# Kernel optimization log

Hardware: AMD Instinct MI355X
Metric: run time of the kernel (lower is better)

Reference implementation:

```python
import jax, jax.numpy as jnp
import numpy as np

B, T, D, K = 8, 1024, 512, 1024
PRECISION = 0.1


def setup_inputs() -> dict:
    key = jax.random.key(0)
    kx, kc = jax.random.split(key)
    x = jax.random.normal(kx, (B, T, D), dtype=jnp.float32)
    codebook = jax.random.normal(kc, (K, D), dtype=jnp.float32)
    precision = PRECISION * jnp.ones((1,), dtype=jnp.float32)
    return {"x": x, "codebook": codebook, "precision": precision}


def reference(x, codebook, precision):
    # score[b,t,k] = -sum_d (x[b,t,d] - codebook[k,d])^2
    x_sq = jnp.sum(x * x, axis=-1, keepdims=True)            # [B,T,1]
    c_sq = jnp.sum(codebook * codebook, axis=-1)              # [K]
    xc = jnp.einsum('btd,kd->btk', x, codebook)               # [B,T,K] GEMM
    score = -(x_sq - 2.0 * xc + c_sq)                         # [B,T,K]
    return precision * score
```

## Files before the change

### kernel.cpp

```cpp
#include <hip/hip_runtime.h>

typedef unsigned short u16;
typedef __attribute__((ext_vector_type(8))) short short8;
typedef __attribute__((ext_vector_type(4))) float f32x4;

typedef void gvoid_t __attribute__((address_space(1)));
typedef void lvoid_t __attribute__((address_space(3)));

#define M_DIM 8192
#define N_DIM 1024
#define K_DIM 512

__device__ __forceinline__ void async_copy16(const void* g, void* l) {
  __builtin_amdgcn_global_load_lds((gvoid_t*)g, (lvoid_t*)l, 16, 0, 0);
}

__device__ __forceinline__ unsigned bf16bits(float v) {
  union { float f; unsigned u; } c; c.f = v;
  return (c.u + 0x7FFFu + ((c.u >> 16) & 1u)) >> 16;
}

__global__ __launch_bounds__(256) void cvt_sq_kernel(
    const float* __restrict__ x, const float* __restrict__ cb,
    u16* __restrict__ xb, u16* __restrict__ cbb,
    float* __restrict__ xsq, float* __restrict__ csq) {
  int row = blockIdx.x * 4 + (threadIdx.x >> 6);
  int lane = threadIdx.x & 63;
  const float* src; u16* dst; float* sq;
  if (row < M_DIM) {
    src = x + (size_t)row * K_DIM; dst = xb + (size_t)row * K_DIM; sq = xsq + row;
  } else {
    int r = row - M_DIM;
    src = cb + (size_t)r * K_DIM; dst = cbb + (size_t)r * K_DIM; sq = csq + r;
  }
  const float4* s4 = (const float4*)src;
  float4 v0 = s4[lane];
  float4 v1 = s4[lane + 64];
  float s = v0.x * v0.x + v0.y * v0.y + v0.z * v0.z + v0.w * v0.w +
            v1.x * v1.x + v1.y * v1.y + v1.z * v1.z + v1.w * v1.w;
  uint2* d2 = (uint2*)dst;
  d2[lane]      = make_uint2(bf16bits(v0.x) | (bf16bits(v0.y) << 16),
                             bf16bits(v0.z) | (bf16bits(v0.w) << 16));
  d2[lane + 64] = make_uint2(bf16bits(v1.x) | (bf16bits(v1.y) << 16),
                             bf16bits(v1.z) | (bf16bits(v1.w) << 16));
#pragma unroll
  for (int off = 32; off > 0; off >>= 1) s += __shfl_xor(s, off, 64);
  if (lane == 0) *sq = s;
}

__global__ __launch_bounds__(256) void qgemm_kernel(
    const u16* __restrict__ A, const u16* __restrict__ B,
    const float* __restrict__ xsq, const float* __restrict__ csq,
    const float* __restrict__ prec, float* __restrict__ out) {
  __shared__ char lds[65536];
  const int tid = threadIdx.x;
  const int wave = tid >> 6, lane = tid & 63;

  const int lin = blockIdx.x;
  const int xcd = lin & 7;
  const int idx = lin >> 3;
  const int ytile = (xcd << 3) | (idx & 7);
  const int xtile = idx >> 3;
  const int m0 = ytile * 128, n0 = xtile * 128;

  const int wm = wave >> 1, wn = wave & 1;
  const int srow = lane >> 3;
  const int scol = ((lane & 7) ^ srow) * 8;
  const int ml = lane & 15, q = lane >> 4;

  auto stage = [&](int k0, int buf) {
    char* base = lds + buf * 32768;
#pragma unroll
    for (int c = wave; c < 16; c += 4) {
      const u16* ga = A + (size_t)(m0 + c * 8 + srow) * K_DIM + (k0 + scol);
      async_copy16(ga, base + c * 1024);
      const u16* gb = B + (size_t)(n0 + c * 8 + srow) * K_DIM + (k0 + scol);
      async_copy16(gb, base + 16384 + c * 1024);
    }
  };

  stage(0, 0);

  const float p = prec[0];
  float csv[4];
#pragma unroll
  for (int j = 0; j < 4; j++) csv[j] = csq[n0 + wn * 64 + j * 16 + ml];

  f32x4 acc[4][4] = {};
  __syncthreads();

  for (int step = 0; step < 8; step++) {
    if (step < 7) stage((step + 1) * 64, (step + 1) & 1);
    const char* base = lds + (step & 1) * 32768;
#pragma unroll
    for (int kk = 0; kk < 2; kk++) {
      const int pcol = ((((kk << 2) | q) ^ (lane & 7)) << 4);
      short8 a[4], b[4];
#pragma unroll
      for (int i = 0; i < 4; i++) {
        a[i] = *(const short8*)(base + (wm * 64 + i * 16 + ml) * 128 + pcol);
        b[i] = *(const short8*)(base + 16384 + (wn * 64 + i * 16 + ml) * 128 + pcol);
      }
#pragma unroll
      for (int i = 0; i < 4; i++)
#pragma unroll
        for (int j = 0; j < 4; j++)
          acc[i][j] = __builtin_amdgcn_mfma_f32_16x16x32_bf16(a[i], b[j], acc[i][j], 0, 0, 0);
    }
    __syncthreads();
  }

#pragma unroll
  for (int i = 0; i < 4; i++) {
#pragma unroll
    for (int r = 0; r < 4; r++) {
      int row = m0 + wm * 64 + i * 16 + q * 4 + r;
      float xs = xsq[row];
      float* orow = out + (size_t)row * N_DIM + n0 + wn * 64 + ml;
#pragma unroll
      for (int j = 0; j < 4; j++)
        __builtin_nontemporal_store(p * (2.0f * acc[i][j][r] - xs - csv[j]),
                                    orow + j * 16);
    }
  }
}

extern "C" void kernel_launch(void* const* d_in, const int* in_sizes, int n_in,
                              void* d_out, int out_size, void* d_ws, size_t ws_size,
                              hipStream_t stream) {
  const float* x    = (const float*)d_in[0];
  const float* cb   = (const float*)d_in[1];
  const float* prec = (const float*)d_in[2];
  float* out = (float*)d_out;

  char* ws = (char*)d_ws;
  u16*   xb  = (u16*)(ws);
  u16*   cbb = (u16*)(ws + 8388608);
  float* xsq = (float*)(ws + 9437184);
  float* csq = (float*)(ws + 9469952);

  cvt_sq_kernel<<<2304, 256, 0, stream>>>(x, cb, xb, cbb, xsq, csq);
  qgemm_kernel<<<512, 256, 0, stream>>>(xb, cbb, xsq, csq, prec, out);
}
```

Measured before the change: 90.37 us.

## Deepen GEMM pipeline to 4-stage ring with BK=32 and explicit vmcnt waits

Replaces the double-buffered BK=64 staging with a four-buffer ring of BK=32 slices, prefetched two steps ahead. Fine-grained s_waitcnt vmcnt plus a raw s_barrier takes the place of __syncthreads. MFMA blocks are wrapped in s_setprio. The aim is to hide global-to-LDS latency better and cut barrier overhead, at the cost of more loop iterations and a subtle ordering dependency on the vmcnt counts. With a distance-2 prefetch into a 4-slot ring there is no write-after-read hazard on the buffers.

```diff
diff --git a/kernel.cpp b/kernel.cpp
--- a/kernel.cpp
+++ b/kernel.cpp
@@ -64,22 +64,26 @@
   const int m0 = ytile * 128, n0 = xtile * 128;
 
   const int wm = wave >> 1, wn = wave & 1;
-  const int srow = lane >> 3;
-  const int scol = ((lane & 7) ^ srow) * 8;
   const int ml = lane & 15, q = lane >> 4;
 
-  auto stage = [&](int k0, int buf) {
-    char* base = lds + buf * 32768;
-#pragma unroll
-    for (int c = wave; c < 16; c += 4) {
-      const u16* ga = A + (size_t)(m0 + c * 8 + srow) * K_DIM + (k0 + scol);
-      async_copy16(ga, base + c * 1024);
-      const u16* gb = B + (size_t)(n0 + c * 8 + srow) * K_DIM + (k0 + scol);
-      async_copy16(gb, base + 16384 + c * 1024);
-    }
+  const int srow = lane >> 2;
+  const int sc = (lane & 3) ^ (srow & 3);
+  const u16* gA0 = A + (size_t)(m0 + wave * 16 + srow) * K_DIM + sc * 8;
+  const u16* gA1 = A + (size_t)(m0 + (wave + 4) * 16 + srow) * K_DIM + sc * 8;
+  const u16* gB0 = B + (size_t)(n0 + wave * 16 + srow) * K_DIM + sc * 8;
+  const u16* gB1 = B + (size_t)(n0 + (wave + 4) * 16 + srow) * K_DIM + sc * 8;
+
+  auto stage = [&](int t) {
+    char* base = lds + ((t & 3) << 14);
+    const int ko = t * 32;
+    async_copy16(gA0 + ko, base + wave * 1024);
+    async_copy16(gA1 + ko, base + (wave + 4) * 1024);
+    async_copy16(gB0 + ko, base + 8192 + wave * 1024);
+    async_copy16(gB1 + ko, base + 8192 + (wave + 4) * 1024);
   };
 
-  stage(0, 0);
+  stage(0);
+  stage(1);
 
   const float p = prec[0];
   float csv[4];
@@ -87,27 +91,34 @@
   for (int j = 0; j < 4; j++) csv[j] = csq[n0 + wn * 64 + j * 16 + ml];
 
   f32x4 acc[4][4] = {};
-  __syncthreads();
+  const int pcol = ((q ^ (ml & 3)) << 4);
 
-  for (int step = 0; step < 8; step++) {
-    if (step < 7) stage((step + 1) * 64, (step + 1) & 1);
-    const char* base = lds + (step & 1) * 32768;
 #pragma unroll
-    for (int kk = 0; kk < 2; kk++) {
-      const int pcol = ((((kk << 2) | q) ^ (lane & 7)) << 4);
-      short8 a[4], b[4];
+  for (int s = 0; s < 16; s++) {
+    if (s < 14) {
+      stage(s + 2);
+      asm volatile("s_waitcnt vmcnt(8)" ::: "memory");
+    } else if (s == 14) {
+      asm volatile("s_waitcnt vmcnt(4)" ::: "memory");
+    } else {
+      asm volatile("s_waitcnt vmcnt(0)" ::: "memory");
+    }
+    __builtin_amdgcn_s_barrier();
+
+    const char* base = lds + ((s & 3) << 14);
+    short8 a[4], b[4];
 #pragma unroll
-      for (int i = 0; i < 4; i++) {
-        a[i] = *(const short8*)(base + (wm * 64 + i * 16 + ml) * 128 + pcol);
-        b[i] = *(const short8*)(base + 16384 + (wn * 64 + i * 16 + ml) * 128 + pcol);
-      }
+    for (int i = 0; i < 4; i++) {
+      a[i] = *(const short8*)(base + (wm * 64 + i * 16 + ml) * 64 + pcol);
+      b[i] = *(const short8*)(base + 8192 + (wn * 64 + i * 16 + ml) * 64 + pcol);
+    }
+    __builtin_amdgcn_s_setprio(1);
 #pragma unroll
-      for (int i = 0; i < 4; i++)
+    for (int i = 0; i < 4; i++)
 #pragma unroll
-        for (int j = 0; j < 4; j++)
-          acc[i][j] = __builtin_amdgcn_mfma_f32_16x16x32_bf16(a[i], b[j], acc[i][j], 0, 0, 0);
-    }
-    __syncthreads();
+      for (int j = 0; j < 4; j++)
+        acc[i][j] = __builtin_amdgcn_mfma_f32_16x16x32_bf16(a[i], b[j], acc[i][j], 0, 0, 0);
+    __builtin_amdgcn_s_setprio(0);
   }
 
 #pragma unroll
```

Measured after the change: 92.08 us. About the same (+1.9%).
